# Kernel optimization log

Measured on AMD Instinct MI355X. Metric: run time of the kernel, lower is better.

Reference implementation:

```python
import jax, jax.numpy as jnp
import numpy as np

EPS = 1e-5  # torch BatchNorm1d default eps


def _project(x, w1, gamma, beta, w2):
    # Linear(bias=False) -> BatchNorm1d (train mode: batch stats, biased var) -> ReLU -> Linear(bias=False)
    h = x @ w1                                   # (n, 128)
    mu = jnp.mean(h, axis=0)
    var = jnp.var(h, axis=0)                     # biased, as torch uses for normalization
    h = (h - mu) * jax.lax.rsqrt(var + EPS) * gamma + beta
    h = jax.nn.relu(h)
    return h @ w2                                # (n, 128)


def setup_inputs() -> dict:
    key = jax.random.key(0)
    k1, k2, k3, k4 = jax.random.split(key, 4)
    latent, hidden = 512, 128
    n_x, n_y = 8192, 2048
    return {
        "variations": jax.random.normal(k1, (n_x, latent), dtype=jnp.float32),
        "exemplar": jax.random.normal(k2, (n_y, latent), dtype=jnp.float32),
        "w1": jax.random.normal(k3, (latent, hidden), dtype=jnp.float32) * (1.0 / np.sqrt(latent)),
        "gamma": jnp.ones((hidden,), dtype=jnp.float32),
        "beta": jnp.zeros((hidden,), dtype=jnp.float32),
        "w2": jax.random.normal(k4, (hidden, hidden), dtype=jnp.float32) * (1.0 / np.sqrt(hidden)),
    }


def reference(variations, exemplar, w1, gamma, beta, w2):
    z1 = _project(variations, w1, gamma, beta, w2)   # (n_x, d)
    z2 = _project(exemplar, w1, gamma, beta, w2)     # (n_y, d)
    # avoids the (n_x, n_y, d) broadcast intermediate of the original)
    x2 = jnp.sum(z1 * z1, axis=1)[:, None]           # (n_x, 1)
    y2 = jnp.sum(z2 * z2, axis=1)[None, :]           # (1, n_y)
    return x2 + y2 - 2.0 * (z1 @ z2.T)               # (n_x, n_y)
```

## Files before the change

### kernel.cpp

```cpp
#include <hip/hip_runtime.h>
#include <hip/hip_bf16.h>


#define LAT 512
#define HID 128
#define EPSV 1e-5f

typedef __attribute__((ext_vector_type(8))) short bf16x8;
typedef __attribute__((ext_vector_type(4))) float f32x4;

__device__ __forceinline__ unsigned short f2bf(float x) {
  unsigned int u = __builtin_bit_cast(unsigned int, x);
  return (unsigned short)((u + 0x7fffu + ((u >> 16) & 1u)) >> 16);
}
__device__ __forceinline__ float bf2f(unsigned short h) {
  unsigned int u = ((unsigned int)h) << 16;
  return __builtin_bit_cast(float, u);
}

__global__ __launch_bounds__(256) void k_prep(const float* __restrict__ W1,
                                              const float* __restrict__ W2,
                                              const float* __restrict__ X1,
                                              const float* __restrict__ X2, int nx,
                                              unsigned short* __restrict__ W1T,
                                              unsigned short* __restrict__ W2T,
                                              unsigned short* __restrict__ Xb) {
  __shared__ float T[64][65];
  const int t = threadIdx.x;
  int bi = blockIdx.x;
  if (bi >= 20) {
    const size_t base = (size_t)(bi - 20) * 2048 + (size_t)t * 8;
    const size_t nxe = (size_t)nx * LAT;
    const float* src = (base < nxe) ? (X1 + base) : (X2 + (base - nxe));
    const float4 a = *(const float4*)src;
    const float4 b = *(const float4*)(src + 4);
    const ushort4 o0 = {f2bf(a.x), f2bf(a.y), f2bf(a.z), f2bf(a.w)};
    const ushort4 o1 = {f2bf(b.x), f2bf(b.y), f2bf(b.z), f2bf(b.w)};
    *(ushort4*)(Xb + base) = o0;
    *(ushort4*)(Xb + base + 4) = o1;
    return;
  }
  const float* src;
  unsigned short* dst;
  int K, N, tk, tn;
  if (bi < 16) { src = W1; dst = W1T; K = LAT; N = HID; tk = bi >> 1; tn = bi & 1; }
  else { bi -= 16; src = W2; dst = W2T; K = HID; N = HID; tk = bi >> 1; tn = bi & 1; }
  const int k0 = tk * 64, n0 = tn * 64;
  {
    const int rr = t >> 4, cc = (t & 15) * 4;
#pragma unroll
    for (int i = 0; i < 4; ++i) {
      const int r = rr + i * 16;
      const float4 v = *(const float4*)(src + (size_t)(k0 + r) * N + n0 + cc);
      T[cc + 0][r] = v.x; T[cc + 1][r] = v.y; T[cc + 2][r] = v.z; T[cc + 3][r] = v.w;
    }
  }
  __syncthreads();
  {
    const int nn = t >> 2, q = (t & 3) * 16;
    unsigned short* dp = dst + (size_t)(n0 + nn) * K + k0 + q;
#pragma unroll
    for (int j = 0; j < 4; ++j) {
      ushort4 o = {f2bf(T[nn][q + j * 4 + 0]), f2bf(T[nn][q + j * 4 + 1]),
                   f2bf(T[nn][q + j * 4 + 2]), f2bf(T[nn][q + j * 4 + 3])};
      *(ushort4*)(dp + j * 4) = o;
    }
  }
}

__global__ __launch_bounds__(256) void k_gemm1(
    const unsigned short* __restrict__ Xb,
    const unsigned short* __restrict__ W1T, unsigned short* __restrict__ H,
    float* __restrict__ pS, float* __restrict__ pQ) {
  __shared__ float sS[16][HID], sQ[16][HID];
  const int tid = threadIdx.x, wid = tid >> 6, lane = tid & 63;
  const int l15 = lane & 15, lq = lane >> 4, lk8 = lq * 8;
  const int row0 = (int)blockIdx.x * 64 + wid * 16;
  const unsigned short* xptr = Xb + (size_t)(row0 + l15) * LAT + lk8;
  f32x4 acc[8];
#pragma unroll
  for (int f = 0; f < 8; ++f) acc[f] = (f32x4){0.f, 0.f, 0.f, 0.f};

#pragma unroll
  for (int kb = 0; kb < LAT; kb += 128) {
    bf16x8 xv[4];
#pragma unroll
    for (int s = 0; s < 4; ++s) xv[s] = *(const bf16x8*)(xptr + kb + s * 32);
#pragma unroll
    for (int s = 0; s < 4; ++s) {
      const int k = kb + s * 32 + lk8;
#pragma unroll
      for (int f = 0; f < 8; ++f) {
        const bf16x8 afr = *(const bf16x8*)(W1T + (size_t)(f * 16 + l15) * LAT + k);
        acc[f] = __builtin_amdgcn_mfma_f32_16x16x32_bf16(afr, xv[s], acc[f], 0, 0, 0);
      }
    }
  }
#pragma unroll
  for (int f = 0; f < 8; ++f) {
    ushort4 hz = {f2bf(acc[f][0]), f2bf(acc[f][1]), f2bf(acc[f][2]), f2bf(acc[f][3])};
    *(ushort4*)(H + (size_t)(row0 + l15) * HID + f * 16 + lq * 4) = hz;
  }
#pragma unroll
  for (int f = 0; f < 8; ++f) {
    f32x4 s = acc[f];
    f32x4 q = acc[f] * acc[f];
#pragma unroll
    for (int r = 0; r < 4; ++r) {
      s[r] += __shfl_xor(s[r], 1, 64);
      q[r] += __shfl_xor(q[r], 1, 64);
      s[r] += __shfl_xor(s[r], 2, 64);
      q[r] += __shfl_xor(q[r], 2, 64);
    }
    if ((l15 & 3) == 0) {
      *(f32x4*)&sS[wid * 4 + (l15 >> 2)][f * 16 + lq * 4] = s;
      *(f32x4*)&sQ[wid * 4 + (l15 >> 2)][f * 16 + lq * 4] = q;
    }
  }
  __syncthreads();
  if (tid < HID) {
    float s = 0.f, q = 0.f;
#pragma unroll
    for (int r = 0; r < 16; ++r) { s += sS[r][tid]; q += sQ[r][tid]; }
    pS[(size_t)blockIdx.x * HID + tid] = s;
    pQ[(size_t)blockIdx.x * HID + tid] = q;
  }
}

__global__ __launch_bounds__(256) void k_gemm2(
    const unsigned short* __restrict__ H,
    const unsigned short* __restrict__ W2T,
    const float* __restrict__ pS, const float* __restrict__ pQ,
    const float* __restrict__ gamma, const float* __restrict__ beta,
    unsigned short* __restrict__ Z, float* __restrict__ nrm,
    int nb1, int nblk, float n1c, float n2c) {
  __shared__ float s_sc[HID], s_sh[HID];
  __shared__ float t0[2][HID], t1[2][HID];
  const int tid = threadIdx.x, wid = tid >> 6, lane = tid & 63;
  const int l15 = lane & 15, lq = lane >> 4, lk8 = lq * 8;
  const bool set1 = (int)blockIdx.x < nb1;
  {
    const int col = tid & 127, half = tid >> 7;
    const int b0 = set1 ? 0 : nb1;
    const int nb = set1 ? nb1 : (nblk - nb1);
    float s = 0.f, q = 0.f;
#pragma unroll 4
    for (int b = half; b < nb; b += 2) {
      s += pS[(size_t)(b0 + b) * HID + col];
      q += pQ[(size_t)(b0 + b) * HID + col];
    }
    t0[half][col] = s;
    t1[half][col] = q;
  }
  __syncthreads();
  if (tid < HID) {
    const float s = t0[0][tid] + t0[1][tid];
    const float q = t1[0][tid] + t1[1][tid];
    const float n = set1 ? n1c : n2c;
    const float mean = s / n;
    const float var = q / n - mean * mean;
    const float rstd = rsqrtf(var + EPSV);
    const float scale = gamma[tid] * rstd;
    s_sc[tid] = scale;
    s_sh[tid] = beta[tid] - mean * scale;
  }
  __syncthreads();
  const int row0 = (int)blockIdx.x * 64 + wid * 16;
  const unsigned short* hptr = H + (size_t)(row0 + l15) * HID + lk8;
  f32x4 acc[8];
#pragma unroll
  for (int f = 0; f < 8; ++f) acc[f] = (f32x4){0.f, 0.f, 0.f, 0.f};
#pragma unroll
  for (int s = 0; s < 4; ++s) {
    const int k = s * 32 + lk8;
    const bf16x8 hv = *(const bf16x8*)(hptr + s * 32);
    const float4 c0 = *(const float4*)&s_sc[k];
    const float4 c1 = *(const float4*)&s_sc[k + 4];
    const float4 d0 = *(const float4*)&s_sh[k];
    const float4 d1 = *(const float4*)&s_sh[k + 4];
    const float cc[8] = {c0.x, c0.y, c0.z, c0.w, c1.x, c1.y, c1.z, c1.w};
    const float dd[8] = {d0.x, d0.y, d0.z, d0.w, d1.x, d1.y, d1.z, d1.w};
    bf16x8 bfr;
#pragma unroll
    for (int i = 0; i < 8; ++i) {
      const float a = fmaxf(fmaf(bf2f((unsigned short)hv[i]), cc[i], dd[i]), 0.f);
      bfr[i] = (short)f2bf(a);
    }
#pragma unroll
    for (int f = 0; f < 8; ++f) {
      const bf16x8 afr = *(const bf16x8*)(W2T + (size_t)(f * 16 + l15) * HID + k);
      acc[f] = __builtin_amdgcn_mfma_f32_16x16x32_bf16(afr, bfr, acc[f], 0, 0, 0);
    }
  }
  float rn = 0.f;
#pragma unroll
  for (int f = 0; f < 8; ++f) {
    rn += acc[f][0] * acc[f][0] + acc[f][1] * acc[f][1] +
          acc[f][2] * acc[f][2] + acc[f][3] * acc[f][3];
    ushort4 z4 = {f2bf(acc[f][0]), f2bf(acc[f][1]), f2bf(acc[f][2]), f2bf(acc[f][3])};
    *(ushort4*)(Z + (size_t)(row0 + l15) * HID + f * 16 + lq * 4) = z4;
  }
  rn += __shfl_xor(rn, 16, 64);
  rn += __shfl_xor(rn, 32, 64);
  if (lane < 16) nrm[row0 + l15] = rn;
}

__global__ __launch_bounds__(256) void k_dist(const unsigned short* __restrict__ Z1b,
                                              const unsigned short* __restrict__ Z2b,
                                              const float* __restrict__ n1,
                                              const float* __restrict__ n2,
                                              float* __restrict__ D, int NY, int ntx) {
  const int nwg = (int)gridDim.x;
  const int cpx = nwg >> 3;
  const int bid = (int)blockIdx.x;
  const int wgid = (bid & 7) * cpx + (bid >> 3);
  const int tby = wgid / ntx, tbx = wgid - tby * ntx;

  const int tid = threadIdx.x;
  const int wid = tid >> 6, lane = tid & 63;
  const int wr = wid >> 1, wc = wid & 1;
  const int rowB = tby * 128 + wr * 64;
  const int colB = tbx * 128 + wc * 64;
  const int l15 = lane & 15, lq = lane >> 4;
  const int lk = lq * 8;
  const unsigned short* Arow = Z1b + (size_t)(rowB + l15) * HID + lk;
  const unsigned short* Brow = Z2b + (size_t)(colB + l15) * HID + lk;
  f32x4 acc[4][4];
#pragma unroll
  for (int i = 0; i < 4; ++i)
#pragma unroll
    for (int j = 0; j < 4; ++j) acc[i][j] = (f32x4){0.f, 0.f, 0.f, 0.f};
#pragma unroll
  for (int s = 0; s < 4; ++s) {
    bf16x8 a[4], b[4];
#pragma unroll
    for (int i = 0; i < 4; ++i) a[i] = *(const bf16x8*)(Arow + (size_t)i * 16 * HID + s * 32);
#pragma unroll
    for (int j = 0; j < 4; ++j) b[j] = *(const bf16x8*)(Brow + (size_t)j * 16 * HID + s * 32);
#pragma unroll
    for (int i = 0; i < 4; ++i)
#pragma unroll
      for (int j = 0; j < 4; ++j)
        acc[i][j] = __builtin_amdgcn_mfma_f32_16x16x32_bf16(b[j], a[i], acc[i][j], 0, 0, 0);
  }
  const int cq = lq * 4;
  float na[4];
#pragma unroll
  for (int i = 0; i < 4; ++i) na[i] = n1[rowB + i * 16 + l15];
#pragma unroll
  for (int j = 0; j < 4; ++j) {
    const float4 nbv = *(const float4*)(n2 + colB + j * 16 + cq);
#pragma unroll
    for (int i = 0; i < 4; ++i) {
      float4 o;
      o.x = na[i] + nbv.x - 2.f * acc[i][j][0];
      o.y = na[i] + nbv.y - 2.f * acc[i][j][1];
      o.z = na[i] + nbv.z - 2.f * acc[i][j][2];
      o.w = na[i] + nbv.w - 2.f * acc[i][j][3];
      *(float4*)(D + (size_t)(rowB + i * 16 + l15) * NY + colB + j * 16 + cq) = o;
    }
  }
}

extern "C" void kernel_launch(void* const* d_in, const int* in_sizes, int n_in,
                              void* d_out, int out_size, void* d_ws, size_t ws_size,
                              hipStream_t stream) {
  const float* variations = (const float*)d_in[0];
  const float* exemplar   = (const float*)d_in[1];
  const float* w1         = (const float*)d_in[2];
  const float* gamma      = (const float*)d_in[3];
  const float* beta       = (const float*)d_in[4];
  const float* w2         = (const float*)d_in[5];
  float* D = (float*)d_out;

  const int nx = in_sizes[0] / LAT;
  const int ny = in_sizes[1] / LAT;
  const int nrows = nx + ny;
  const int nbb = nrows / 64;
  const int nb1 = nx / 64;

  char* p = (char*)d_ws;
  unsigned short* Xb  = (unsigned short*)p; p += (size_t)nrows * LAT * 2;
  unsigned short* Hb  = (unsigned short*)p; p += (size_t)nrows * HID * 2;
  unsigned short* Zb  = (unsigned short*)p; p += (size_t)nrows * HID * 2;
  unsigned short* W1T = (unsigned short*)p; p += (size_t)LAT * HID * 2;
  unsigned short* W2T = (unsigned short*)p; p += (size_t)HID * HID * 2;
  float* pS = (float*)p;  p += (size_t)nbb * HID * 4;
  float* pQ = (float*)p;  p += (size_t)nbb * HID * 4;
  float* nrmAll = (float*)p; p += (size_t)nrows * 4;
  float* n1v = nrmAll;
  float* n2v = nrmAll + nx;
  unsigned short* Z1b = Zb;
  unsigned short* Z2b = Zb + (size_t)nx * HID;

  const int xblocks = (nrows * LAT) / 2048;
  k_prep<<<20 + xblocks, 256, 0, stream>>>(w1, w2, variations, exemplar, nx,
                                           W1T, W2T, Xb);
  k_gemm1<<<nbb, 256, 0, stream>>>(Xb, W1T, Hb, pS, pQ);
  k_gemm2<<<nbb, 256, 0, stream>>>(Hb, W2T, pS, pQ, gamma, beta, Zb, nrmAll,
                                   nb1, nbb, (float)nx, (float)ny);
  const int ntx = ny / 128;
  const int nwg = (nx / 128) * ntx;
  k_dist<<<nwg, 256, 0, stream>>>(Z1b, Z2b, n1v, n2v, D, ny, ntx);
}
```

Baseline: 67.72 us.

## Pre-pack X and W1 into MFMA fragment order for coalesced GEMM1 loads

New measurement: 62.58 us. 1.08x faster.

```diff
diff --git a/kernel.cpp b/kernel.cpp
--- a/kernel.cpp
+++ b/kernel.cpp
@@ -22,9 +22,9 @@
                                               const float* __restrict__ W2,
                                               const float* __restrict__ X1,
                                               const float* __restrict__ X2, int nx,
-                                              unsigned short* __restrict__ W1T,
+                                              unsigned short* __restrict__ W1P,
                                               unsigned short* __restrict__ W2T,
-                                              unsigned short* __restrict__ Xb) {
+                                              unsigned short* __restrict__ XbP) {
   __shared__ float T[64][65];
   const int t = threadIdx.x;
   int bi = blockIdx.x;
@@ -34,66 +34,97 @@
     const float* src = (base < nxe) ? (X1 + base) : (X2 + (base - nxe));
     const float4 a = *(const float4*)src;
     const float4 b = *(const float4*)(src + 4);
+    const int row = (int)(base >> 9);
+    const int k = (int)(base & 511);
+    const int st = row >> 4, l15 = row & 15;
+    const int tf = k >> 5, lq = (k >> 3) & 3;
+    const size_t off = ((((size_t)st * 16 + tf) * 16 + l15) * 4 + lq) * 8;
     const ushort4 o0 = {f2bf(a.x), f2bf(a.y), f2bf(a.z), f2bf(a.w)};
     const ushort4 o1 = {f2bf(b.x), f2bf(b.y), f2bf(b.z), f2bf(b.w)};
-    *(ushort4*)(Xb + base) = o0;
-    *(ushort4*)(Xb + base + 4) = o1;
+    *(ushort4*)(XbP + off) = o0;
+    *(ushort4*)(XbP + off + 4) = o1;
     return;
   }
-  const float* src;
-  unsigned short* dst;
-  int K, N, tk, tn;
-  if (bi < 16) { src = W1; dst = W1T; K = LAT; N = HID; tk = bi >> 1; tn = bi & 1; }
-  else { bi -= 16; src = W2; dst = W2T; K = HID; N = HID; tk = bi >> 1; tn = bi & 1; }
-  const int k0 = tk * 64, n0 = tn * 64;
-  {
-    const int rr = t >> 4, cc = (t & 15) * 4;
-#pragma unroll
-    for (int i = 0; i < 4; ++i) {
-      const int r = rr + i * 16;
-      const float4 v = *(const float4*)(src + (size_t)(k0 + r) * N + n0 + cc);
-      T[cc + 0][r] = v.x; T[cc + 1][r] = v.y; T[cc + 2][r] = v.z; T[cc + 3][r] = v.w;
-    }
-  }
-  __syncthreads();
-  {
-    const int nn = t >> 2, q = (t & 3) * 16;
-    unsigned short* dp = dst + (size_t)(n0 + nn) * K + k0 + q;
-#pragma unroll
-    for (int j = 0; j < 4; ++j) {
-      ushort4 o = {f2bf(T[nn][q + j * 4 + 0]), f2bf(T[nn][q + j * 4 + 1]),
-                   f2bf(T[nn][q + j * 4 + 2]), f2bf(T[nn][q + j * 4 + 3])};
-      *(ushort4*)(dp + j * 4) = o;
+  if (bi < 16) {
+    const int tk = bi >> 1, tn = bi & 1;
+    const int k0 = tk * 64, n0 = tn * 64;
+    {
+      const int rr = t >> 4, cc = (t & 15) * 4;
+#pragma unroll
+      for (int i = 0; i < 4; ++i) {
+        const int r = rr + i * 16;
+        const float4 v = *(const float4*)(W1 + (size_t)(k0 + r) * HID + n0 + cc);
+        T[cc + 0][r] = v.x; T[cc + 1][r] = v.y; T[cc + 2][r] = v.z; T[cc + 3][r] = v.w;
+      }
+    }
+    __syncthreads();
+    {
+      const int nn = t >> 2, q = (t & 3) * 16;
+      const int n = n0 + nn;
+      const int f = n >> 4, l15 = n & 15;
+#pragma unroll
+      for (int e8 = 0; e8 < 2; ++e8) {
+        const int kq = q + e8 * 8;
+        const int kk = k0 + kq;
+        const int tf = kk >> 5, lq = (kk >> 3) & 3;
+        const size_t off = ((((size_t)f * 16 + tf) * 16 + l15) * 4 + lq) * 8;
+        const ushort4 lo = {f2bf(T[nn][kq + 0]), f2bf(T[nn][kq + 1]),
+                            f2bf(T[nn][kq + 2]), f2bf(T[nn][kq + 3])};
+        const ushort4 hi = {f2bf(T[nn][kq + 4]), f2bf(T[nn][kq + 5]),
+                            f2bf(T[nn][kq + 6]), f2bf(T[nn][kq + 7])};
+        *(ushort4*)(W1P + off) = lo;
+        *(ushort4*)(W1P + off + 4) = hi;
+      }
+    }
+  } else {
+    bi -= 16;
+    const int tk = bi >> 1, tn = bi & 1;
+    const int k0 = tk * 64, n0 = tn * 64;
+    {
+      const int rr = t >> 4, cc = (t & 15) * 4;
+#pragma unroll
+      for (int i = 0; i < 4; ++i) {
+        const int r = rr + i * 16;
+        const float4 v = *(const float4*)(W2 + (size_t)(k0 + r) * HID + n0 + cc);
+        T[cc + 0][r] = v.x; T[cc + 1][r] = v.y; T[cc + 2][r] = v.z; T[cc + 3][r] = v.w;
+      }
+    }
+    __syncthreads();
+    {
+      const int nn = t >> 2, q = (t & 3) * 16;
+      unsigned short* dp = W2T + (size_t)(n0 + nn) * HID + k0 + q;
+#pragma unroll
+      for (int j = 0; j < 4; ++j) {
+        ushort4 o = {f2bf(T[nn][q + j * 4 + 0]), f2bf(T[nn][q + j * 4 + 1]),
+                     f2bf(T[nn][q + j * 4 + 2]), f2bf(T[nn][q + j * 4 + 3])};
+        *(ushort4*)(dp + j * 4) = o;
+      }
     }
   }
 }
 
 __global__ __launch_bounds__(256) void k_gemm1(
-    const unsigned short* __restrict__ Xb,
-    const unsigned short* __restrict__ W1T, unsigned short* __restrict__ H,
+    const unsigned short* __restrict__ XbP,
+    const unsigned short* __restrict__ W1P, unsigned short* __restrict__ H,
     float* __restrict__ pS, float* __restrict__ pQ) {
   __shared__ float sS[16][HID], sQ[16][HID];
   const int tid = threadIdx.x, wid = tid >> 6, lane = tid & 63;
-  const int l15 = lane & 15, lq = lane >> 4, lk8 = lq * 8;
+  const int l15 = lane & 15, lq = lane >> 4;
   const int row0 = (int)blockIdx.x * 64 + wid * 16;
-  const unsigned short* xptr = Xb + (size_t)(row0 + l15) * LAT + lk8;
+  const int st = row0 >> 4;
+  const unsigned short* xp = XbP + (((size_t)st * 16 * 16 + l15) * 4 + lq) * 8;
+  const unsigned short* wp = W1P + (((size_t)l15) * 4 + lq) * 8;
   f32x4 acc[8];
 #pragma unroll
   for (int f = 0; f < 8; ++f) acc[f] = (f32x4){0.f, 0.f, 0.f, 0.f};
 
 #pragma unroll
-  for (int kb = 0; kb < LAT; kb += 128) {
-    bf16x8 xv[4];
-#pragma unroll
-    for (int s = 0; s < 4; ++s) xv[s] = *(const bf16x8*)(xptr + kb + s * 32);
-#pragma unroll
-    for (int s = 0; s < 4; ++s) {
-      const int k = kb + s * 32 + lk8;
-#pragma unroll
-      for (int f = 0; f < 8; ++f) {
-        const bf16x8 afr = *(const bf16x8*)(W1T + (size_t)(f * 16 + l15) * LAT + k);
-        acc[f] = __builtin_amdgcn_mfma_f32_16x16x32_bf16(afr, xv[s], acc[f], 0, 0, 0);
-      }
+  for (int t = 0; t < 16; ++t) {
+    const bf16x8 xv = *(const bf16x8*)(xp + (size_t)t * 512);
+#pragma unroll
+    for (int f = 0; f < 8; ++f) {
+      const bf16x8 afr = *(const bf16x8*)(wp + (size_t)(f * 16 + t) * 512);
+      acc[f] = __builtin_amdgcn_mfma_f32_16x16x32_bf16(afr, xv, acc[f], 0, 0, 0);
     }
   }
 #pragma unroll
@@ -280,10 +311,10 @@
   const int nb1 = nx / 64;
 
   char* p = (char*)d_ws;
-  unsigned short* Xb  = (unsigned short*)p; p += (size_t)nrows * LAT * 2;
+  unsigned short* XbP = (unsigned short*)p; p += (size_t)nrows * LAT * 2;
   unsigned short* Hb  = (unsigned short*)p; p += (size_t)nrows * HID * 2;
   unsigned short* Zb  = (unsigned short*)p; p += (size_t)nrows * HID * 2;
-  unsigned short* W1T = (unsigned short*)p; p += (size_t)LAT * HID * 2;
+  unsigned short* W1P = (unsigned short*)p; p += (size_t)LAT * HID * 2;
   unsigned short* W2T = (unsigned short*)p; p += (size_t)HID * HID * 2;
   float* pS = (float*)p;  p += (size_t)nbb * HID * 4;
   float* pQ = (float*)p;  p += (size_t)nbb * HID * 4;
@@ -295,8 +326,8 @@
 
   const int xblocks = (nrows * LAT) / 2048;
   k_prep<<<20 + xblocks, 256, 0, stream>>>(w1, w2, variations, exemplar, nx,
-                                           W1T, W2T, Xb);
-  k_gemm1<<<nbb, 256, 0, stream>>>(Xb, W1T, Hb, pS, pQ);
+                                           W1P, W2T, XbP);
+  k_gemm1<<<nbb, 256, 0, stream>>>(XbP, W1P, Hb, pS, pQ);
   k_gemm2<<<nbb, 256, 0, stream>>>(Hb, W2T, pS, pQ, gamma, beta, Zb, nrmAll,
                                    nb1, nbb, (float)nx, (float)ny);
   const int ntx = ny / 128;
```
